# Optimization experiments

Measured on AMD Instinct MI355X. Metric: run time of the kernel, lower is better.

Reference implementation:

```python
import jax, jax.numpy as jnp
import numpy as np

B, S, H = 4, 4096, 2048
NH = 16
HD = H // NH  # 128


def setup_inputs() -> dict:
    key = jax.random.key(0)
    ks = jax.random.split(key, 11)
    scale = 1.0 / np.sqrt(H)
    inp = {"hidden_states": jax.random.normal(ks[0], (B, S, H), dtype=jnp.float32)}
    names = ["q", "k", "v", "g", "o"]
    for i, n in enumerate(names):
        inp[f"W{n}"] = jax.random.uniform(ks[1 + i], (H, H), dtype=jnp.float32, minval=-scale, maxval=scale)
        inp[f"b{n}"] = jax.random.uniform(ks[6 + i], (H,), dtype=jnp.float32, minval=-scale, maxval=scale)
    return inp


def reference(hidden_states, Wq, bq, Wk, bk, Wv, bv, Wg, bg, Wo, bo):
    x = hidden_states
    b, s, _ = x.shape

    def heads(t):  # [b,s,H] -> [b,nh,s,hd]
        return t.reshape(b, s, NH, HD).transpose(0, 2, 1, 3)

    q = heads(x @ Wq + bq)
    k = heads(x @ Wk + bk)
    v = heads(x @ Wv + bv)
    g = heads(jax.nn.sigmoid(x @ Wg + bg))
    # kv state: [b,h,d,e]; small per-head outer-product sum over seq
    kv = jnp.einsum('bhsd,bhse->bhde', k, v)
    out = jnp.einsum('bhsd,bhde->bhse', q, kv)
    out = (out * g).transpose(0, 2, 1, 3).reshape(b, s, -1)
    return out @ Wo + bo
```

## Files before the change

kernel.cpp:

```cpp
#include <hip/hip_runtime.h>
#include <stdint.h>

typedef unsigned short u16;
typedef unsigned int   u32;
typedef __bf16 bf16x8 __attribute__((ext_vector_type(8)));
typedef float  f32x4  __attribute__((ext_vector_type(4)));
typedef u16    u16x8  __attribute__((ext_vector_type(8)));
typedef u16    u16x4  __attribute__((ext_vector_type(4)));

#define NB    4
#define NS    4096
#define NHID  2048
#define NHEAD 16
#define HDIM  128
#define NKT   32

__device__ __forceinline__ u16 f2bf(float f) {
  u32 u = __builtin_bit_cast(u32, f);
  u = (u + 0x7fffu + ((u >> 16) & 1u)) >> 16;
  return (u16)u;
}
__device__ __forceinline__ float bf2f(u16 h) {
  return __builtin_bit_cast(float, ((u32)h) << 16);
}

__device__ __forceinline__ void async_copy16(u16* lds_dst, const u16* g_src) {
  __builtin_amdgcn_global_load_lds(
      (__attribute__((address_space(1))) u32*)(const_cast<u16*>(g_src)),
      (__attribute__((address_space(3))) u32*)(lds_dst),
      16, 0, 0);
}

#define SBAR()  __builtin_amdgcn_sched_barrier(0)
#define BARRIER() do { SBAR(); __builtin_amdgcn_s_barrier(); SBAR(); } while (0)
#define LGKM0() asm volatile("s_waitcnt lgkmcnt(0)" ::: "memory")
#define VM0()   asm volatile("s_waitcnt vmcnt(0)"   ::: "memory")
#define VM4()   asm volatile("s_waitcnt vmcnt(4)"   ::: "memory")

__device__ __forceinline__ void stage10(u16* dst, const u16* src,
                                        int kt, int kg, int tid)
{
#pragma unroll
  for (int i = 0; i < 2; ++i) {
    const int U = (i << 9) + tid;
    const int r = U >> 2, u = U & 3;
    const int col = (kt << 6) + (kg << 5) + ((u ^ ((r >> 1) & 3)) << 3);
    async_copy16(dst + U * 8, src + (size_t)r * 2048 + col);
  }
}

__device__ __forceinline__ void rdA(bf16x8 (&d)[4], const u16* base, int mq)
{
#pragma unroll
  for (int m = 0; m < 4; ++m)
    d[m] = *(const bf16x8*)(base + mq * 2048 + m * 512);
}

__device__ __forceinline__ void rdB(bf16x8 (&d)[4], const u16* base)
{
#pragma unroll
  for (int n = 0; n < 4; ++n)
    d[n] = *(const bf16x8*)(base + n * 512);
}

template<bool SWAP>
__device__ __forceinline__ void mmcl(f32x4 (&acc)[8][4], int mq,
                                     const bf16x8 (&a)[4], const bf16x8 (&b)[4])
{
  __builtin_amdgcn_s_setprio(1);
#pragma unroll
  for (int mm = 0; mm < 4; ++mm)
#pragma unroll
    for (int n = 0; n < 4; ++n) {
      if (SWAP)
        acc[mq * 4 + mm][n] = __builtin_amdgcn_mfma_f32_16x16x32_bf16(b[n], a[mm], acc[mq * 4 + mm][n], 0, 0, 0);
      else
        acc[mq * 4 + mm][n] = __builtin_amdgcn_mfma_f32_16x16x32_bf16(a[mm], b[n], acc[mq * 4 + mm][n], 0, 0, 0);
    }
  __builtin_amdgcn_s_setprio(0);
}

template<bool SWAP>
__device__ __forceinline__ void gemm10(const u16* __restrict__ A,
                                       const u16* __restrict__ B,
                                       f32x4 (&acc)[8][4], u16* L)
{
  const int tid = threadIdx.x, lane = tid & 63, w = tid >> 6;
  const int wr = w >> 2, wc = w & 3, lg = lane >> 4, lr = lane & 15;
  const int ggx = ((lg ^ ((lr >> 1) & 3)) << 3);
  const int arow = wr * 4096 + lr * 32 + ggx;
  const int brow = wc * 2048 + lr * 32 + ggx;

#pragma unroll
  for (int m = 0; m < 8; ++m)
#pragma unroll
    for (int n = 0; n < 4; ++n) acc[m][n] = f32x4{0.f, 0.f, 0.f, 0.f};

  stage10(L,         A, 0, 0, tid);
  stage10(L + 16384, B, 0, 0, tid);
  SBAR();
  stage10(L + 8192,  A, 0, 1, tid);
  stage10(L + 24576, B, 0, 1, tid);
  VM0();
  BARRIER();

  bf16x8 aRa[4], aRb[4], bR0[4], bR1[4];
  rdA(aRa, L + arow, 0);
  rdB(bR0, L + 16384 + brow);
  LGKM0();

#pragma unroll 1
  for (int t = 0; t < NKT - 1; ++t) {
    u16* Lc = L + ((t & 1) << 15);
    u16* Ln = L + (((t + 1) & 1) << 15);
    stage10(Ln,         A, t + 1, 0, tid);
    stage10(Ln + 16384, B, t + 1, 0, tid);
    VM4();
    BARRIER();
    rdA(aRb, Lc + arow, 1);
    mmcl<SWAP>(acc, 0, aRa, bR0);
    LGKM0();
    stage10(Ln + 8192,  A, t + 1, 1, tid);
    stage10(Ln + 24576, B, t + 1, 1, tid);
    BARRIER();
    rdA(aRa, Lc + 8192 + arow, 0);
    rdB(bR1, Lc + 24576 + brow);
    mmcl<SWAP>(acc, 1, aRb, bR0);
    LGKM0();
    BARRIER();
    rdA(aRb, Lc + 8192 + arow, 1);
    mmcl<SWAP>(acc, 0, aRa, bR1);
    LGKM0();
    VM4();
    BARRIER();
    rdA(aRa, Ln + arow, 0);
    rdB(bR0, Ln + 16384 + brow);
    mmcl<SWAP>(acc, 1, aRb, bR1);
    LGKM0();
  }
  {
    u16* Lc = L + (((NKT - 1) & 1) << 15);
    VM0();
    BARRIER();
    rdA(aRb, Lc + arow, 1);
    mmcl<SWAP>(acc, 0, aRa, bR0);
    LGKM0();
    BARRIER();
    rdA(aRa, Lc + 8192 + arow, 0);
    rdB(bR1, Lc + 24576 + brow);
    mmcl<SWAP>(acc, 1, aRb, bR0);
    LGKM0();
    BARRIER();
    rdA(aRb, Lc + 8192 + arow, 1);
    mmcl<SWAP>(acc, 0, aRa, bR1);
    LGKM0();
    BARRIER();
    mmcl<SWAP>(acc, 1, aRb, bR1);
  }
}

__global__ __launch_bounds__(512, 2) void k_gemm_qkvg(
    const u16* __restrict__ xb, const u16* __restrict__ WT,
    const float* __restrict__ bias,
    u16* __restrict__ q, u16* __restrict__ kT, u16* __restrict__ vT,
    u16* __restrict__ g)
{
  __shared__ u16 L[65536];
  const int bid = blockIdx.x;
  const int grp = bid >> 8, r = bid & 255;
  const int mt = ((grp & 3) << 4) + (r & 15);
  const int nt = ((grp >> 2) << 4) + (r >> 4);
  const size_t bm0 = (size_t)mt << 8;
  const int    bn0 = nt << 8;
  const int nblk = bn0 >> 11;
  const int ocol0 = bn0 & 2047;

  const int tid = threadIdx.x, lane = tid & 63, w = tid >> 6;
  const int wr = w >> 2, wc = w & 3, lg = lane >> 4, lr = lane & 15;

  f32x4 acc[8][4];
  const u16* Ap = xb + bm0 * NHID;
  const u16* Bp = WT + (size_t)bn0 * NHID;

  if (nblk == 0 || nblk == 3) {
    gemm10<true>(Ap, Bp, acc, L);
    u16* outp = (nblk == 0) ? q : g;
    const bool sig = (nblk == 3);
#pragma unroll
    for (int m = 0; m < 8; ++m) {
      const size_t row = bm0 + (wr << 7) + (m << 4) + lr;
#pragma unroll
      for (int n = 0; n < 4; ++n) {
        const int colb = (wc << 6) + (n << 4) + (lg << 2);
        const float* bp = bias + bn0 + colb;
        u16x4 o;
#pragma unroll
        for (int j = 0; j < 4; ++j) {
          float val = acc[m][n][j] + bp[j];
          if (sig) val = 1.f / (1.f + __expf(-val));
          o[j] = f2bf(val);
        }
        *(u16x4*)(outp + row * NHID + ocol0 + colb) = o;
      }
    }
  } else {
    gemm10<false>(Ap, Bp, acc, L);
    u16* outp = (nblk == 1) ? kT : vT;
    const int b = (int)(bm0 >> 12);
    const int srow0 = (int)(bm0 & 4095) + (wr << 7) + (lg << 2);
#pragma unroll
    for (int m = 0; m < 8; ++m) {
      const int srow = srow0 + (m << 4);
#pragma unroll
      for (int n = 0; n < 4; ++n) {
        const int cg = ocol0 + (wc << 6) + (n << 4) + lr;
        const int h = cg >> 7, d = cg & 127;
        const float bia = bias[bn0 + (wc << 6) + (n << 4) + lr];
        u16x4 o;
#pragma unroll
        for (int j = 0; j < 4; ++j) o[j] = f2bf(acc[m][n][j] + bia);
        *(u16x4*)(outp + (((size_t)(b * NHEAD + h) * HDIM + d) << 12) + srow) = o;
      }
    }
  }
}

__global__ __launch_bounds__(512, 2) void k_gemm_out(
    const u16* __restrict__ attn, const u16* __restrict__ WoT,
    const float* __restrict__ bo, float* __restrict__ out)
{
  __shared__ u16 L[65536];
  const int bid = blockIdx.x;
  const int grp = bid >> 7, rr = bid & 127;
  const int mt = (grp << 4) + (rr & 15);
  const int nt = rr >> 4;
  const size_t bm0 = (size_t)mt << 8;
  const int    bn0 = nt << 8;

  const int tid = threadIdx.x, lane = tid & 63, w = tid >> 6;
  const int wr = w >> 2, wc = w & 3, lg = lane >> 4, lr = lane & 15;

  f32x4 acc[8][4];
  gemm10<true>(attn + bm0 * NHID, WoT + (size_t)bn0 * NHID, acc, L);

#pragma unroll
  for (int m = 0; m < 8; ++m) {
    const size_t row = bm0 + (wr << 7) + (m << 4) + lr;
#pragma unroll
    for (int n = 0; n < 4; ++n) {
      const int colb = bn0 + (wc << 6) + (n << 4) + (lg << 2);
      f32x4 o;
#pragma unroll
      for (int j = 0; j < 4; ++j) o[j] = acc[m][n][j] + bo[colb + j];
      *(f32x4*)(out + row * NHID + colb) = o;
    }
  }
}

__device__ __forceinline__ void gemm_core(const u16* A, int lda,
                                          const u16* B, int ldb,
                                          int K, f32x4 acc[4][4],
                                          u16* As, u16* Bs)
{
  const int tid  = threadIdx.x;
  const int lane = tid & 63;
  const int w    = tid >> 6;
  const int wr   = (w >> 1) << 6;
  const int wc   = (w & 1) << 6;
  const int lg   = lane >> 4;
  const int lr   = lane & 15;

#pragma unroll
  for (int m = 0; m < 4; ++m)
#pragma unroll
    for (int n = 0; n < 4; ++n) acc[m][n] = f32x4{0.f, 0.f, 0.f, 0.f};

  for (int k0 = 0; k0 < K; k0 += 32) {
#pragma unroll
    for (int issue = 0; issue < 2; ++issue) {
      int c   = issue * 256 + tid;
      int row = c >> 2, cc = (c & 3) << 3;
      async_copy16(As + c * 8, A + (size_t)row * lda + k0 + cc);
    }
#pragma unroll
    for (int issue = 0; issue < 2; ++issue) {
      int c   = issue * 256 + tid;
      int row = c >> 2, cc = (c & 3) << 3;
      async_copy16(Bs + c * 8, B + (size_t)row * ldb + k0 + cc);
    }
    __syncthreads();

    bf16x8 af[4], bv[4];
#pragma unroll
    for (int m = 0; m < 4; ++m)
      af[m] = *(const bf16x8*)(As + ((wr + m * 16 + lr) << 5) + (lg << 3));
#pragma unroll
    for (int n = 0; n < 4; ++n)
      bv[n] = *(const bf16x8*)(Bs + ((wc + n * 16 + lr) << 5) + (lg << 3));

#pragma unroll
    for (int m = 0; m < 4; ++m)
#pragma unroll
      for (int n = 0; n < 4; ++n)
        acc[m][n] = __builtin_amdgcn_mfma_f32_16x16x32_bf16(af[m], bv[n], acc[m][n], 0, 0, 0);

    __syncthreads();
  }
}

__global__ __launch_bounds__(256) void k_gemm_kv(
    const u16* __restrict__ vT, const u16* __restrict__ kT, float* __restrict__ part)
{
  __shared__ u16 As[128 * 32];
  __shared__ u16 Bs[128 * 32];
  const int bh = blockIdx.x, sp = blockIdx.y;
  const u16* A  = vT + (size_t)bh * (HDIM * NS) + sp * 512;
  const u16* Bt = kT + (size_t)bh * (HDIM * NS) + sp * 512;
  f32x4 acc[4][4];
  gemm_core(A, NS, Bt, NS, 512, acc, As, Bs);

  float* outp = part + ((size_t)sp * 64 + bh) * 16384;
  const int tid = threadIdx.x, lane = tid & 63, w = tid >> 6;
  const int wr = (w >> 1) << 6, wc = (w & 1) << 6, lg = lane >> 4, lr = lane & 15;
#pragma unroll
  for (int m = 0; m < 4; ++m)
#pragma unroll
    for (int n = 0; n < 4; ++n) {
      const int col = wc + n * 16 + lr;
#pragma unroll
      for (int j = 0; j < 4; ++j) {
        const int row = wr + m * 16 + lg * 4 + j;
        outp[row * 128 + col] = acc[m][n][j];
      }
    }
}

__global__ __launch_bounds__(256) void k_gemm_attn(
    const u16* __restrict__ q, const u16* __restrict__ kvT,
    const u16* __restrict__ g, u16* __restrict__ attn)
{
  __shared__ u16 As[128 * 32];
  __shared__ u16 Bs[128 * 32];
  const int st = blockIdx.x, bh = blockIdx.y;
  const int b = bh >> 4, h = bh & 15;
  const size_t bs0 = (size_t)b * NS + st * 128;
  f32x4 acc[4][4];
  gemm_core(q + bs0 * NHID + h * HDIM, NHID, kvT + (size_t)bh * 16384, HDIM, HDIM, acc, As, Bs);

  const int tid = threadIdx.x, lane = tid & 63, w = tid >> 6;
  const int wr = (w >> 1) << 6, wc = (w & 1) << 6, lg = lane >> 4, lr = lane & 15;
#pragma unroll
  for (int m = 0; m < 4; ++m)
#pragma unroll
    for (int n = 0; n < 4; ++n) {
      const int col = wc + n * 16 + lr;
#pragma unroll
      for (int j = 0; j < 4; ++j) {
        const int row = wr + m * 16 + lg * 4 + j;
        const size_t idx = (bs0 + row) * NHID + h * HDIM + col;
        attn[idx] = f2bf(acc[m][n][j] * bf2f(g[idx]));
      }
    }
}

__global__ __launch_bounds__(256) void k_cvt_x(const float* __restrict__ x, u16* __restrict__ xb)
{
  const size_t i = (size_t)blockIdx.x * 256 + threadIdx.x;
  const float4* xf = (const float4*)x;
  float4 a = xf[2 * i];
  float4 b = xf[2 * i + 1];
  u16x8 o;
  o[0] = f2bf(a.x); o[1] = f2bf(a.y); o[2] = f2bf(a.z); o[3] = f2bf(a.w);
  o[4] = f2bf(b.x); o[5] = f2bf(b.y); o[6] = f2bf(b.z); o[7] = f2bf(b.w);
  ((u16x8*)xb)[i] = o;
}

__global__ __launch_bounds__(256) void k_cvt_w_t(const float* __restrict__ W, u16* __restrict__ WT)
{
  __shared__ u16 t[64][72];
  const int kt = blockIdx.x, nt = blockIdx.y;
  const int tid = threadIdx.x;
#pragma unroll
  for (int pass = 0; pass < 4; ++pass) {
    int c = pass * 256 + tid;
    int r = c >> 4, cc = (c & 15) << 2;
    float4 vv = *(const float4*)(W + (size_t)(kt * 64 + r) * 2048 + nt * 64 + cc);
    u16x4 o;
    o[0] = f2bf(vv.x); o[1] = f2bf(vv.y); o[2] = f2bf(vv.z); o[3] = f2bf(vv.w);
    *(u16x4*)&t[r][cc] = o;
  }
  __syncthreads();
#pragma unroll
  for (int pass = 0; pass < 2; ++pass) {
    int c = pass * 256 + tid;
    int rn = c >> 3, cs = (c & 7) << 3;
    u16x8 o;
#pragma unroll
    for (int j = 0; j < 8; ++j) o[j] = t[cs + j][rn];
    *(u16x8*)(WT + (size_t)(nt * 64 + rn) * 2048 + kt * 64 + cs) = o;
  }
}

__global__ __launch_bounds__(256) void k_bias_cat(
    const float* __restrict__ bq, const float* __restrict__ bk,
    const float* __restrict__ bv, const float* __restrict__ bg, float* __restrict__ o)
{
  const int i = blockIdx.x * 256 + threadIdx.x;
  const int blk = i >> 11;
  const float* s = (blk == 0) ? bq : (blk == 1) ? bk : (blk == 2) ? bv : bg;
  o[i] = s[i & 2047];
}

__global__ __launch_bounds__(256) void k_kv_reduce(const float* __restrict__ part, u16* __restrict__ kvT)
{
  const int i = blockIdx.x * 256 + threadIdx.x;
  float s = 0.f;
#pragma unroll
  for (int sp = 0; sp < 8; ++sp) s += part[(size_t)sp * 1048576 + i];
  kvT[i] = f2bf(s);
}

extern "C" void kernel_launch(void* const* d_in, const int* in_sizes, int n_in,
                              void* d_out, int out_size, void* d_ws, size_t ws_size,
                              hipStream_t stream)
{
  const float* x  = (const float*)d_in[0];
  const float* Wq = (const float*)d_in[1];
  const float* bq = (const float*)d_in[2];
  const float* Wk = (const float*)d_in[3];
  const float* bk = (const float*)d_in[4];
  const float* Wv = (const float*)d_in[5];
  const float* bv = (const float*)d_in[6];
  const float* Wg = (const float*)d_in[7];
  const float* bg = (const float*)d_in[8];
  const float* Wo = (const float*)d_in[9];
  const float* bo = (const float*)d_in[10];
  float* out = (float*)d_out;

  char* ws = (char*)d_ws;
  u16*   xb   = (u16*)(ws + 0x00000000ULL);
  u16*   WT   = (u16*)(ws + 0x04000000ULL);
  u16*   WoT  = (u16*)(ws + 0x06000000ULL);
  float* bias = (float*)(ws + 0x06800000ULL);
  u16*   q    = (u16*)(ws + 0x06900000ULL);
  u16*   kT   = (u16*)(ws + 0x0A900000ULL);
  u16*   vT   = (u16*)(ws + 0x0E900000ULL);
  u16*   gg   = (u16*)(ws + 0x12900000ULL);
  u16*   kvT  = (u16*)(ws + 0x16900000ULL);
  float* part = (float*)WT;
  u16*   attn = xb;

  if (ws_size < 0x16B00000ULL) return;

  k_cvt_x<<<16384, 256, 0, stream>>>(x, xb);
  k_cvt_w_t<<<dim3(32, 32), 256, 0, stream>>>(Wq, WT);
  k_cvt_w_t<<<dim3(32, 32), 256, 0, stream>>>(Wk, WT + (size_t)2048 * 2048);
  k_cvt_w_t<<<dim3(32, 32), 256, 0, stream>>>(Wv, WT + (size_t)2 * 2048 * 2048);
  k_cvt_w_t<<<dim3(32, 32), 256, 0, stream>>>(Wg, WT + (size_t)3 * 2048 * 2048);
  k_cvt_w_t<<<dim3(32, 32), 256, 0, stream>>>(Wo, WoT);
  k_bias_cat<<<32, 256, 0, stream>>>(bq, bk, bv, bg, bias);

  k_gemm_qkvg<<<2048, 512, 0, stream>>>(xb, WT, bias, q, kT, vT, gg);

  k_gemm_kv<<<dim3(64, 8), 256, 0, stream>>>(vT, kT, part);
  k_kv_reduce<<<4096, 256, 0, stream>>>(part, kvT);

  k_gemm_attn<<<dim3(32, 64), 256, 0, stream>>>(q, kvT, gg, attn);
  k_gemm_out<<<512, 512, 0, stream>>>(attn, WoT, bo, out);
}
```

Before: 878.6 us.

## Restructure GEMM main loop into four barrier-delimited phases and merge weight conversions

Replaces the software-pipelined GEMM inner loop, which double-buffered register fragments and interleaved staging, with a four-phase scheme. Each phase reads LDS fragments, issues one quarter of the next tile's async copies, waits, hits a barrier, then runs the MFMA cluster between barriers. The aim is to spread global-to-LDS traffic evenly and cut register pressure by using one set of A/B fragments instead of two. The cost is that LDS reads no longer overlap with MFMA work and there are more barriers per tile. Separately, the five weight transpose-convert launches are merged into one 3D-grid launch to cut launch overhead.

```diff
diff --git a/kernel.cpp b/kernel.cpp
--- a/kernel.cpp
+++ b/kernel.cpp
@@ -35,7 +35,6 @@
 #define BARRIER() do { SBAR(); __builtin_amdgcn_s_barrier(); SBAR(); } while (0)
 #define LGKM0() asm volatile("s_waitcnt lgkmcnt(0)" ::: "memory")
 #define VM0()   asm volatile("s_waitcnt vmcnt(0)"   ::: "memory")
-#define VM4()   asm volatile("s_waitcnt vmcnt(4)"   ::: "memory")
 
 __device__ __forceinline__ void stage10(u16* dst, const u16* src,
                                         int kt, int kg, int tid)
@@ -80,8 +79,36 @@
   __builtin_amdgcn_s_setprio(0);
 }
 
+template<int Q, int VMW, bool STG, bool SWAP>
+__device__ __forceinline__ void phase14(const u16* Lc, u16* Ln,
+                                        const u16* __restrict__ A,
+                                        const u16* __restrict__ B, int ktn,
+                                        bf16x8 (&aR)[4], bf16x8 (&bR)[4],
+                                        f32x4 (&acc)[8][4],
+                                        int tid, int arow, int brow)
+{
+  if (Q == 0) { rdB(bR, Lc + 16384 + brow); rdA(aR, Lc + arow, 0); }
+  if (Q == 1) { rdA(aR, Lc + arow, 1); }
+  if (Q == 2) { rdB(bR, Lc + 24576 + brow); rdA(aR, Lc + 8192 + arow, 0); }
+  if (Q == 3) { rdA(aR, Lc + 8192 + arow, 1); }
+  if (STG) {
+    if (Q == 0) stage10(Ln,         A, ktn, 0, tid);
+    if (Q == 1) stage10(Ln + 16384, B, ktn, 0, tid);
+    if (Q == 2) stage10(Ln + 8192,  A, ktn, 1, tid);
+    if (Q == 3) stage10(Ln + 24576, B, ktn, 1, tid);
+  }
+  if constexpr (VMW >= 0) {
+    asm volatile("s_waitcnt vmcnt(%0)" :: "n"(VMW) : "memory");
+  }
+  BARRIER();
+  LGKM0();
+  SBAR();
+  mmcl<SWAP>(acc, (Q & 1), aR, bR);
+  BARRIER();
+}
+
 template<bool SWAP>
-__device__ __forceinline__ void gemm10(const u16* __restrict__ A,
+__device__ __forceinline__ void gemm14(const u16* __restrict__ A,
                                        const u16* __restrict__ B,
                                        f32x4 (&acc)[8][4], u16* L)
 {
@@ -98,64 +125,27 @@
 
   stage10(L,         A, 0, 0, tid);
   stage10(L + 16384, B, 0, 0, tid);
-  SBAR();
   stage10(L + 8192,  A, 0, 1, tid);
   stage10(L + 24576, B, 0, 1, tid);
   VM0();
   BARRIER();
 
-  bf16x8 aRa[4], aRb[4], bR0[4], bR1[4];
-  rdA(aRa, L + arow, 0);
-  rdB(bR0, L + 16384 + brow);
-  LGKM0();
-
+  bf16x8 aR[4], bR[4];
 #pragma unroll 1
   for (int t = 0; t < NKT - 1; ++t) {
-    u16* Lc = L + ((t & 1) << 15);
+    const u16* Lc = L + ((t & 1) << 15);
     u16* Ln = L + (((t + 1) & 1) << 15);
-    stage10(Ln,         A, t + 1, 0, tid);
-    stage10(Ln + 16384, B, t + 1, 0, tid);
-    VM4();
-    BARRIER();
-    rdA(aRb, Lc + arow, 1);
-    mmcl<SWAP>(acc, 0, aRa, bR0);
-    LGKM0();
-    stage10(Ln + 8192,  A, t + 1, 1, tid);
-    stage10(Ln + 24576, B, t + 1, 1, tid);
-    BARRIER();
-    rdA(aRa, Lc + 8192 + arow, 0);
-    rdB(bR1, Lc + 24576 + brow);
-    mmcl<SWAP>(acc, 1, aRb, bR0);
-    LGKM0();
-    BARRIER();
-    rdA(aRb, Lc + 8192 + arow, 1);
-    mmcl<SWAP>(acc, 0, aRa, bR1);
-    LGKM0();
-    VM4();
-    BARRIER();
-    rdA(aRa, Ln + arow, 0);
-    rdB(bR0, Ln + 16384 + brow);
-    mmcl<SWAP>(acc, 1, aRb, bR1);
-    LGKM0();
+    phase14<0, -1, true, SWAP>(Lc, Ln, A, B, t + 1, aR, bR, acc, tid, arow, brow);
+    phase14<1,  4, true, SWAP>(Lc, Ln, A, B, t + 1, aR, bR, acc, tid, arow, brow);
+    phase14<2, -1, true, SWAP>(Lc, Ln, A, B, t + 1, aR, bR, acc, tid, arow, brow);
+    phase14<3,  4, true, SWAP>(Lc, Ln, A, B, t + 1, aR, bR, acc, tid, arow, brow);
   }
   {
-    u16* Lc = L + (((NKT - 1) & 1) << 15);
-    VM0();
-    BARRIER();
-    rdA(aRb, Lc + arow, 1);
-    mmcl<SWAP>(acc, 0, aRa, bR0);
-    LGKM0();
-    BARRIER();
-    rdA(aRa, Lc + 8192 + arow, 0);
-    rdB(bR1, Lc + 24576 + brow);
-    mmcl<SWAP>(acc, 1, aRb, bR0);
-    LGKM0();
-    BARRIER();
-    rdA(aRb, Lc + 8192 + arow, 1);
-    mmcl<SWAP>(acc, 0, aRa, bR1);
-    LGKM0();
-    BARRIER();
-    mmcl<SWAP>(acc, 1, aRb, bR1);
+    const u16* Lc = L + (((NKT - 1) & 1) << 15);
+    phase14<0, -1, false, SWAP>(Lc, nullptr, A, B, 0, aR, bR, acc, tid, arow, brow);
+    phase14<1,  0, false, SWAP>(Lc, nullptr, A, B, 0, aR, bR, acc, tid, arow, brow);
+    phase14<2, -1, false, SWAP>(Lc, nullptr, A, B, 0, aR, bR, acc, tid, arow, brow);
+    phase14<3, -1, false, SWAP>(Lc, nullptr, A, B, 0, aR, bR, acc, tid, arow, brow);
   }
 }
 
@@ -183,7 +173,7 @@
   const u16* Bp = WT + (size_t)bn0 * NHID;
 
   if (nblk == 0 || nblk == 3) {
-    gemm10<true>(Ap, Bp, acc, L);
+    gemm14<true>(Ap, Bp, acc, L);
     u16* outp = (nblk == 0) ? q : g;
     const bool sig = (nblk == 3);
 #pragma unroll
@@ -204,7 +194,7 @@
       }
     }
   } else {
-    gemm10<false>(Ap, Bp, acc, L);
+    gemm14<false>(Ap, Bp, acc, L);
     u16* outp = (nblk == 1) ? kT : vT;
     const int b = (int)(bm0 >> 12);
     const int srow0 = (int)(bm0 & 4095) + (wr << 7) + (lg << 2);
@@ -241,7 +231,7 @@
   const int wr = w >> 2, wc = w & 3, lg = lane >> 4, lr = lane & 15;
 
   f32x4 acc[8][4];
-  gemm10<true>(attn + bm0 * NHID, WoT + (size_t)bn0 * NHID, acc, L);
+  gemm14<true>(attn + bm0 * NHID, WoT + (size_t)bn0 * NHID, acc, L);
 
 #pragma unroll
   for (int m = 0; m < 8; ++m) {
@@ -375,10 +365,17 @@
   ((u16x8*)xb)[i] = o;
 }
 
-__global__ __launch_bounds__(256) void k_cvt_w_t(const float* __restrict__ W, u16* __restrict__ WT)
+__global__ __launch_bounds__(256) void k_cvt_w_t5(
+    const float* __restrict__ Wq, const float* __restrict__ Wk,
+    const float* __restrict__ Wv, const float* __restrict__ Wg,
+    const float* __restrict__ Wo,
+    u16* __restrict__ WT, u16* __restrict__ WoT)
 {
   __shared__ u16 t[64][72];
-  const int kt = blockIdx.x, nt = blockIdx.y;
+  const int kt = blockIdx.x, nt = blockIdx.y, z = blockIdx.z;
+  const float* W = (z == 0) ? Wq : (z == 1) ? Wk : (z == 2) ? Wv
+                 : (z == 3) ? Wg : Wo;
+  u16* dst = (z == 4) ? WoT : (WT + (size_t)z * 2048 * 2048);
   const int tid = threadIdx.x;
 #pragma unroll
   for (int pass = 0; pass < 4; ++pass) {
@@ -397,7 +394,7 @@
     u16x8 o;
 #pragma unroll
     for (int j = 0; j < 8; ++j) o[j] = t[cs + j][rn];
-    *(u16x8*)(WT + (size_t)(nt * 64 + rn) * 2048 + kt * 64 + cs) = o;
+    *(u16x8*)(dst + (size_t)(nt * 64 + rn) * 2048 + kt * 64 + cs) = o;
   }
 }
 
@@ -453,11 +450,7 @@
   if (ws_size < 0x16B00000ULL) return;
 
   k_cvt_x<<<16384, 256, 0, stream>>>(x, xb);
-  k_cvt_w_t<<<dim3(32, 32), 256, 0, stream>>>(Wq, WT);
-  k_cvt_w_t<<<dim3(32, 32), 256, 0, stream>>>(Wk, WT + (size_t)2048 * 2048);
-  k_cvt_w_t<<<dim3(32, 32), 256, 0, stream>>>(Wv, WT + (size_t)2 * 2048 * 2048);
-  k_cvt_w_t<<<dim3(32, 32), 256, 0, stream>>>(Wg, WT + (size_t)3 * 2048 * 2048);
-  k_cvt_w_t<<<dim3(32, 32), 256, 0, stream>>>(Wo, WoT);
+  k_cvt_w_t5<<<dim3(32, 32, 5), 256, 0, stream>>>(Wq, Wk, Wv, Wg, Wo, WT, WoT);
   k_bias_cat<<<32, 256, 0, stream>>>(bq, bk, bv, bg, bias);
 
   k_gemm_qkvg<<<2048, 512, 0, stream>>>(xb, WT, bias, q, kT, vT, gg);
```

New measurement: 818.0 us. 1.07x faster.
